# Kernel optimization log

Hardware: AMD Instinct MI355X
Metric: run time of the kernel (lower is better)

The kernel has to match this reference:

```python
import jax, jax.numpy as jnp
import numpy as np

SCALE = 30.0  # self.s


def setup_inputs() -> dict:
    key = jax.random.key(0)
    x = jax.random.normal(key, (2048, 8, 128), dtype=jnp.float32)
    return {"x": x}


def reference(x):
    # x: [S, G, d] = [stepsize (speakers), gsize (utts/speaker), embed dim]
    S, G, d = x.shape
    # F.normalize(x, p=2, dim=2)
    xn = x / jnp.clip(jnp.linalg.norm(x, axis=2, keepdims=True), 1e-12)
    centroids = xn.mean(axis=1)  # [S, d]
    # exclusive centroids: mean over the G-1 other utterances, for every ii at once
    exc = (xn.sum(axis=1, keepdims=True) - xn) / (G - 1)  # [S, G, d]
    exc_n = exc / jnp.clip(jnp.linalg.norm(exc, axis=2, keepdims=True), 1e-8)
    # xn rows are unit norm, so cosine_similarity = dot with normalized exc
    cosine_exc = jnp.sum(xn * exc_n, axis=2)  # [S, G]
    # NOTE: in the source, one_hot = zeros then scatter_(0) stays all-zero, so the
    # ArcFace phi branch contributes nothing: output == cosine_exc exactly.
    cent_n = centroids / jnp.clip(jnp.linalg.norm(centroids, axis=1, keepdims=True), 1e-8)
    # full similarity of every utterance against every centroid: [S, G, S]
    cos_sim = SCALE * jnp.einsum('sgd,td->sgt', xn, cent_n)
    # replace diagonal (own-speaker entry) with exclusive-centroid similarity
    diag = jnp.arange(S)
    cos_sim = cos_sim.at[diag, :, diag].set(SCALE * cosine_exc)
    # torch.clamp(cos_sim, 1e-06) clamps min only
    logits = jnp.clip(cos_sim, 1e-6).reshape(S * G, S)
    labels = jnp.repeat(jnp.arange(S), G)  # repeat_interleave(arange(S), G)
    logp = jax.nn.log_softmax(logits, axis=-1)
    nloss = -jnp.mean(logp[jnp.arange(S * G), labels])
    return nloss
```

## Files before the change

kernel.cpp:

```cpp
#include <hip/hip_runtime.h>
#include <hip/hip_bf16.h>

#define S_DIM 2048
#define G_DIM 8
#define D_DIM 128
#define N_ROWS (S_DIM * G_DIM)
#define SCALE 30.0f
#define NSPLIT 16
#define TCHUNK (S_DIM / NSPLIT)

typedef __attribute__((ext_vector_type(8))) short bf16x8;
typedef __attribute__((ext_vector_type(4))) float f32x4;

__device__ __forceinline__ float wave_allreduce_sum(float v) {
    #pragma unroll
    for (int m = 32; m >= 1; m >>= 1) v += __shfl_xor(v, m, 64);
    return v;
}

__global__ __launch_bounds__(512) void prep_kernel(
    const float* __restrict__ x,
    __hip_bfloat16* __restrict__ xnb,
    __hip_bfloat16* __restrict__ centb,
    float* __restrict__ cosexc)
{
    __shared__ float xs[G_DIM][D_DIM];
    __shared__ float csum[D_DIM];

    const int s    = blockIdx.x;
    const int g    = threadIdx.x >> 6;
    const int lane = threadIdx.x & 63;
    const int d0 = lane, d1 = lane + 64;

    const float* xr = x + (s * G_DIM + g) * D_DIM;
    float a0 = xr[d0], a1 = xr[d1];

    float ss  = wave_allreduce_sum(a0 * a0 + a1 * a1);
    float inv = 1.0f / fmaxf(sqrtf(ss), 1e-12f);
    float x0 = a0 * inv, x1 = a1 * inv;

    xs[g][d0] = x0;
    xs[g][d1] = x1;
    __hip_bfloat16* xw = xnb + (s * G_DIM + g) * D_DIM;
    xw[d0] = __float2bfloat16(x0);
    xw[d1] = __float2bfloat16(x1);
    __syncthreads();

    if (threadIdx.x < D_DIM) {
        float c = 0.0f;
        #pragma unroll
        for (int gg = 0; gg < G_DIM; ++gg) c += xs[gg][threadIdx.x];
        csum[threadIdx.x] = c;
    }
    __syncthreads();

    float e0 = (csum[d0] - x0) * (1.0f / (G_DIM - 1));
    float e1 = (csum[d1] - x1) * (1.0f / (G_DIM - 1));
    float ess = wave_allreduce_sum(e0 * e0 + e1 * e1);
    float ed  = fmaxf(sqrtf(ess), 1e-8f);
    float dot = wave_allreduce_sum(x0 * e0 + x1 * e1);
    if (lane == 0) cosexc[s * G_DIM + g] = dot / ed;

    if (g == 0) {
        float c0 = csum[d0], c1 = csum[d1];
        float css  = wave_allreduce_sum(c0 * c0 + c1 * c1);
        float cnrm = sqrtf(css) * (1.0f / G_DIM);
        float scl  = (1.0f / G_DIM) / fmaxf(cnrm, 1e-8f);
        centb[s * D_DIM + d0] = __float2bfloat16(c0 * scl);
        centb[s * D_DIM + d1] = __float2bfloat16(c1 * scl);
    }
}

__global__ __launch_bounds__(256, 4) void score_kernel(
    const __hip_bfloat16* __restrict__ xnb,
    const __hip_bfloat16* __restrict__ centb,
    const float* __restrict__ cosexc,
    float* __restrict__ psum,
    float* __restrict__ plab)
{
    const int wave  = threadIdx.x >> 6;
    const int lane  = threadIdx.x & 63;
    const int row0  = (blockIdx.x * 4 + wave) * 64;
    const int split = blockIdx.y;
    const int tbase = split * TCHUNK;
    const int nIdx  = lane & 15;
    const int quad  = lane >> 4;
    const int s0    = row0 >> 3;

    const short* xsrc = (const short*)xnb;
    bf16x8 afrag[4][4];
    #pragma unroll
    for (int m = 0; m < 4; ++m) {
        const int abase = (row0 + m * 16 + nIdx) * D_DIM + quad * 8;
        #pragma unroll
        for (int kc = 0; kc < 4; ++kc)
            afrag[m][kc] = *(const bf16x8*)(xsrc + abase + kc * 32);
    }

    float sumexp[4][4];
    #pragma unroll
    for (int m = 0; m < 4; ++m)
        #pragma unroll
        for (int r = 0; r < 4; ++r) sumexp[m][r] = 0.0f;

    const short* csrc = (const short*)centb;
    for (int t0 = tbase; t0 < tbase + TCHUNK; t0 += 16) {
        bf16x8 bfrag[4];
        const int bbase = (t0 + nIdx) * D_DIM + quad * 8;
        #pragma unroll
        for (int kc = 0; kc < 4; ++kc)
            bfrag[kc] = *(const bf16x8*)(csrc + bbase + kc * 32);

        f32x4 acc[4];
        #pragma unroll
        for (int m = 0; m < 4; ++m) acc[m] = (f32x4){0.f, 0.f, 0.f, 0.f};
        #pragma unroll
        for (int kc = 0; kc < 4; ++kc)
            #pragma unroll
            for (int m = 0; m < 4; ++m)
                acc[m] = __builtin_amdgcn_mfma_f32_16x16x32_bf16(
                    afrag[m][kc], bfrag[kc], acc[m], 0, 0, 0);

        const int t = t0 + nIdx;
        if (t0 <= s0 + 7 && t0 + 16 > s0) {
            #pragma unroll
            for (int m = 0; m < 4; ++m) {
                #pragma unroll
                for (int r = 0; r < 4; ++r) {
                    const int grow = row0 + m * 16 + quad * 4 + r;
                    float l = fmaxf(SCALE * acc[m][r], 1e-6f);
                    if (t == (grow >> 3)) {
                        l = fmaxf(SCALE * cosexc[grow], 1e-6f);
                        plab[grow] = l;
                    }
                    sumexp[m][r] += __expf(l - SCALE);
                }
            }
        } else {
            #pragma unroll
            for (int m = 0; m < 4; ++m) {
                #pragma unroll
                for (int r = 0; r < 4; ++r) {
                    float l = fmaxf(SCALE * acc[m][r], 1e-6f);
                    sumexp[m][r] += __expf(l - SCALE);
                }
            }
        }
    }

    #pragma unroll
    for (int m = 0; m < 4; ++m) {
        #pragma unroll
        for (int r = 0; r < 4; ++r) {
            #pragma unroll
            for (int msk = 1; msk <= 8; msk <<= 1)
                sumexp[m][r] += __shfl_xor(sumexp[m][r], msk, 64);
        }
    }
    if (nIdx == 0) {
        #pragma unroll
        for (int m = 0; m < 4; ++m)
            #pragma unroll
            for (int r = 0; r < 4; ++r)
                psum[split * N_ROWS + row0 + m * 16 + quad * 4 + r] = sumexp[m][r];
    }
}

__global__ __launch_bounds__(256) void combine_kernel(
    const float* __restrict__ psum, const float* __restrict__ plab,
    float* __restrict__ out)
{
    __shared__ float red[4];
    const int row = blockIdx.x * 256 + threadIdx.x;

    float s = 0.0f;
    #pragma unroll
    for (int j = 0; j < NSPLIT; ++j) s += psum[j * N_ROWS + row];
    float loss = SCALE + logf(s) - plab[row];

    float v = wave_allreduce_sum(loss);
    const int wave = threadIdx.x >> 6;
    if ((threadIdx.x & 63) == 0) red[wave] = v;
    __syncthreads();
    if (threadIdx.x == 0)
        atomicAdd(out, (red[0] + red[1] + red[2] + red[3]) * (1.0f / N_ROWS));
}

extern "C" void kernel_launch(void* const* d_in, const int* in_sizes, int n_in,
                              void* d_out, int out_size, void* d_ws, size_t ws_size,
                              hipStream_t stream) {
    const float* x = (const float*)d_in[0];
    char* ws = (char*)d_ws;

    size_t off = 0;
    __hip_bfloat16* xnb   = (__hip_bfloat16*)(ws + off); off += (size_t)N_ROWS * D_DIM * 2;
    __hip_bfloat16* centb = (__hip_bfloat16*)(ws + off); off += (size_t)S_DIM * D_DIM * 2;
    float* cosexc = (float*)(ws + off); off += (size_t)N_ROWS * 4;
    float* psum   = (float*)(ws + off); off += (size_t)NSPLIT * N_ROWS * 4;
    float* plab   = (float*)(ws + off); off += (size_t)N_ROWS * 4;
    float* out = (float*)d_out;

    hipMemsetAsync(out, 0, sizeof(float), stream);
    prep_kernel<<<S_DIM, 512, 0, stream>>>(x, xnb, centb, cosexc);
    score_kernel<<<dim3(N_ROWS / 256, NSPLIT), 256, 0, stream>>>(xnb, centb, cosexc, psum, plab);
    combine_kernel<<<N_ROWS / 256, 256, 0, stream>>>(psum, plab, out);
}
```

Measured before the change: 91.96 us.

## Fuse row normalization into score kernel and replace atomic loss reduction

The score kernel now loads raw fp32 inputs, computes each row's L2 norm with cross-lane shuffles and converts to bf16 in registers. This removes the normalized bf16 intermediate written by the prep kernel. The final loss is reduced through per-block partial sums and a single-wave finalize kernel instead of a memset plus atomicAdd. In exchange, each split re-reads fp32 rows, doubling A-operand bytes, and the normalization is recomputed for every split.

```diff
diff --git a/kernel.cpp b/kernel.cpp
--- a/kernel.cpp
+++ b/kernel.cpp
@@ -18,9 +18,13 @@
     return v;
 }
 
+__device__ __forceinline__ short f2bf(float f) {
+    __hip_bfloat16 h = __float2bfloat16(f);
+    return *reinterpret_cast<short*>(&h);
+}
+
 __global__ __launch_bounds__(512) void prep_kernel(
     const float* __restrict__ x,
-    __hip_bfloat16* __restrict__ xnb,
     __hip_bfloat16* __restrict__ centb,
     float* __restrict__ cosexc)
 {
@@ -41,9 +45,6 @@
 
     xs[g][d0] = x0;
     xs[g][d1] = x1;
-    __hip_bfloat16* xw = xnb + (s * G_DIM + g) * D_DIM;
-    xw[d0] = __float2bfloat16(x0);
-    xw[d1] = __float2bfloat16(x1);
     __syncthreads();
 
     if (threadIdx.x < D_DIM) {
@@ -72,7 +73,7 @@
 }
 
 __global__ __launch_bounds__(256, 4) void score_kernel(
-    const __hip_bfloat16* __restrict__ xnb,
+    const float* __restrict__ x,
     const __hip_bfloat16* __restrict__ centb,
     const float* __restrict__ cosexc,
     float* __restrict__ psum,
@@ -87,14 +88,33 @@
     const int quad  = lane >> 4;
     const int s0    = row0 >> 3;
 
-    const short* xsrc = (const short*)xnb;
     bf16x8 afrag[4][4];
     #pragma unroll
     for (int m = 0; m < 4; ++m) {
-        const int abase = (row0 + m * 16 + nIdx) * D_DIM + quad * 8;
-        #pragma unroll
-        for (int kc = 0; kc < 4; ++kc)
-            afrag[m][kc] = *(const bf16x8*)(xsrc + abase + kc * 32);
+        const float* xr = x + (size_t)(row0 + m * 16 + nIdx) * D_DIM + quad * 8;
+        float4 va[4], vb[4];
+        float ss = 0.0f;
+        #pragma unroll
+        for (int kc = 0; kc < 4; ++kc) {
+            va[kc] = *(const float4*)(xr + kc * 32);
+            vb[kc] = *(const float4*)(xr + kc * 32 + 4);
+            ss += va[kc].x * va[kc].x + va[kc].y * va[kc].y
+                + va[kc].z * va[kc].z + va[kc].w * va[kc].w
+                + vb[kc].x * vb[kc].x + vb[kc].y * vb[kc].y
+                + vb[kc].z * vb[kc].z + vb[kc].w * vb[kc].w;
+        }
+        ss += __shfl_xor(ss, 16, 64);
+        ss += __shfl_xor(ss, 32, 64);
+        const float inv = 1.0f / fmaxf(sqrtf(ss), 1e-12f);
+        #pragma unroll
+        for (int kc = 0; kc < 4; ++kc) {
+            bf16x8 t;
+            t[0] = f2bf(va[kc].x * inv); t[1] = f2bf(va[kc].y * inv);
+            t[2] = f2bf(va[kc].z * inv); t[3] = f2bf(va[kc].w * inv);
+            t[4] = f2bf(vb[kc].x * inv); t[5] = f2bf(vb[kc].y * inv);
+            t[6] = f2bf(vb[kc].z * inv); t[7] = f2bf(vb[kc].w * inv);
+            afrag[m][kc] = t;
+        }
     }
 
     float sumexp[4][4];
@@ -168,7 +188,7 @@
 
 __global__ __launch_bounds__(256) void combine_kernel(
     const float* __restrict__ psum, const float* __restrict__ plab,
-    float* __restrict__ out)
+    float* __restrict__ bsum)
 {
     __shared__ float red[4];
     const int row = blockIdx.x * 256 + threadIdx.x;
@@ -183,7 +203,15 @@
     if ((threadIdx.x & 63) == 0) red[wave] = v;
     __syncthreads();
     if (threadIdx.x == 0)
-        atomicAdd(out, (red[0] + red[1] + red[2] + red[3]) * (1.0f / N_ROWS));
+        bsum[blockIdx.x] = red[0] + red[1] + red[2] + red[3];
+}
+
+__global__ __launch_bounds__(64) void finalize_kernel(
+    const float* __restrict__ bsum, float* __restrict__ out)
+{
+    float v = bsum[threadIdx.x];
+    v = wave_allreduce_sum(v);
+    if (threadIdx.x == 0) out[0] = v * (1.0f / N_ROWS);
 }
 
 extern "C" void kernel_launch(void* const* d_in, const int* in_sizes, int n_in,
@@ -193,15 +221,15 @@
     char* ws = (char*)d_ws;
 
     size_t off = 0;
-    __hip_bfloat16* xnb   = (__hip_bfloat16*)(ws + off); off += (size_t)N_ROWS * D_DIM * 2;
     __hip_bfloat16* centb = (__hip_bfloat16*)(ws + off); off += (size_t)S_DIM * D_DIM * 2;
     float* cosexc = (float*)(ws + off); off += (size_t)N_ROWS * 4;
     float* psum   = (float*)(ws + off); off += (size_t)NSPLIT * N_ROWS * 4;
     float* plab   = (float*)(ws + off); off += (size_t)N_ROWS * 4;
+    float* bsum   = (float*)(ws + off); off += 64 * 4;
     float* out = (float*)d_out;
 
-    hipMemsetAsync(out, 0, sizeof(float), stream);
-    prep_kernel<<<S_DIM, 512, 0, stream>>>(x, xnb, centb, cosexc);
-    score_kernel<<<dim3(N_ROWS / 256, NSPLIT), 256, 0, stream>>>(xnb, centb, cosexc, psum, plab);
-    combine_kernel<<<N_ROWS / 256, 256, 0, stream>>>(psum, plab, out);
-}
+    prep_kernel<<<S_DIM, 512, 0, stream>>>(x, centb, cosexc);
+    score_kernel<<<dim3(N_ROWS / 256, NSPLIT), 256, 0, stream>>>(x, centb, cosexc, psum, plab);
+    combine_kernel<<<N_ROWS / 256, 256, 0, stream>>>(psum, plab, bsum);
+    finalize_kernel<<<1, 64, 0, stream>>>(bsum, out);
+}
```

Result: slower. 100.8 us (+9.6%).

## Prefetch centroid fragments and replace memset+atomic with a finalize kernel

Applied to the files above, without the earlier changes.

The score kernel now double-buffers the B (centroid) fragments, loading the next 16-centroid tile while MFMAs and exp work run on the current one. Launch bounds drop from 4 to 3 waves per SIMD to make room for the extra registers. The combine stage writes per-block partial sums, and a new single-wave finalize kernel reduces them. This removes the memset and the atomicAdd but adds one more kernel launch.

```diff
diff --git a/kernel.cpp b/kernel.cpp
--- a/kernel.cpp
+++ b/kernel.cpp
@@ -71,7 +71,7 @@
     }
 }
 
-__global__ __launch_bounds__(256, 4) void score_kernel(
+__global__ __launch_bounds__(256, 3) void score_kernel(
     const __hip_bfloat16* __restrict__ xnb,
     const __hip_bfloat16* __restrict__ centb,
     const float* __restrict__ cosexc,
@@ -83,6 +83,7 @@
     const int row0  = (blockIdx.x * 4 + wave) * 64;
     const int split = blockIdx.y;
     const int tbase = split * TCHUNK;
+    const int tend  = tbase + TCHUNK;
     const int nIdx  = lane & 15;
     const int quad  = lane >> 4;
     const int s0    = row0 >> 3;
@@ -104,12 +105,21 @@
         for (int r = 0; r < 4; ++r) sumexp[m][r] = 0.0f;
 
     const short* csrc = (const short*)centb;
-    for (int t0 = tbase; t0 < tbase + TCHUNK; t0 += 16) {
-        bf16x8 bfrag[4];
-        const int bbase = (t0 + nIdx) * D_DIM + quad * 8;
-        #pragma unroll
-        for (int kc = 0; kc < 4; ++kc)
-            bfrag[kc] = *(const bf16x8*)(csrc + bbase + kc * 32);
+
+    bf16x8 bcur[4], bnxt[4];
+    {
+        const int bbase = (tbase + nIdx) * D_DIM + quad * 8;
+        #pragma unroll
+        for (int kc = 0; kc < 4; ++kc)
+            bcur[kc] = *(const bf16x8*)(csrc + bbase + kc * 32);
+    }
+
+    for (int t0 = tbase; t0 < tend; t0 += 16) {
+        const int tn = (t0 + 16 < tend) ? (t0 + 16) : tbase;
+        const int nbase = (tn + nIdx) * D_DIM + quad * 8;
+        #pragma unroll
+        for (int kc = 0; kc < 4; ++kc)
+            bnxt[kc] = *(const bf16x8*)(csrc + nbase + kc * 32);
 
         f32x4 acc[4];
         #pragma unroll
@@ -119,7 +129,7 @@
             #pragma unroll
             for (int m = 0; m < 4; ++m)
                 acc[m] = __builtin_amdgcn_mfma_f32_16x16x32_bf16(
-                    afrag[m][kc], bfrag[kc], acc[m], 0, 0, 0);
+                    afrag[m][kc], bcur[kc], acc[m], 0, 0, 0);
 
         const int t = t0 + nIdx;
         if (t0 <= s0 + 7 && t0 + 16 > s0) {
@@ -146,6 +156,9 @@
                 }
             }
         }
+
+        #pragma unroll
+        for (int kc = 0; kc < 4; ++kc) bcur[kc] = bnxt[kc];
     }
 
     #pragma unroll
@@ -168,7 +181,7 @@
 
 __global__ __launch_bounds__(256) void combine_kernel(
     const float* __restrict__ psum, const float* __restrict__ plab,
-    float* __restrict__ out)
+    float* __restrict__ bsum)
 {
     __shared__ float red[4];
     const int row = blockIdx.x * 256 + threadIdx.x;
@@ -183,7 +196,15 @@
     if ((threadIdx.x & 63) == 0) red[wave] = v;
     __syncthreads();
     if (threadIdx.x == 0)
-        atomicAdd(out, (red[0] + red[1] + red[2] + red[3]) * (1.0f / N_ROWS));
+        bsum[blockIdx.x] = red[0] + red[1] + red[2] + red[3];
+}
+
+__global__ __launch_bounds__(64) void finalize_kernel(
+    const float* __restrict__ bsum, float* __restrict__ out)
+{
+    float v = bsum[threadIdx.x];
+    v = wave_allreduce_sum(v);
+    if (threadIdx.x == 0) out[0] = v * (1.0f / N_ROWS);
 }
 
 extern "C" void kernel_launch(void* const* d_in, const int* in_sizes, int n_in,
@@ -198,10 +219,11 @@
     float* cosexc = (float*)(ws + off); off += (size_t)N_ROWS * 4;
     float* psum   = (float*)(ws + off); off += (size_t)NSPLIT * N_ROWS * 4;
     float* plab   = (float*)(ws + off); off += (size_t)N_ROWS * 4;
+    float* bsum   = (float*)(ws + off); off += 64 * 4;
     float* out = (float*)d_out;
 
-    hipMemsetAsync(out, 0, sizeof(float), stream);
     prep_kernel<<<S_DIM, 512, 0, stream>>>(x, xnb, centb, cosexc);
     score_kernel<<<dim3(N_ROWS / 256, NSPLIT), 256, 0, stream>>>(xnb, centb, cosexc, psum, plab);
-    combine_kernel<<<N_ROWS / 256, 256, 0, stream>>>(psum, plab, out);
-}
+    combine_kernel<<<N_ROWS / 256, 256, 0, stream>>>(psum, plab, bsum);
+    finalize_kernel<<<1, 64, 0, stream>>>(bsum, out);
+}
```

Measured after the change: 96.15 us. 1.05x slower.
